# Performance work log

Hardware: AMD Instinct MI355X
Metric: run time of the kernel (lower is better)

Reference implementation:

```python
import jax, jax.numpy as jnp
import numpy as np

B, S, D_MODEL, N_HEADS = 2, 2048, 2048, 16
D_K = D_MODEL // N_HEADS
MAX_SEQ_LEN = 4096


def _rope_tables(seq_len, d_k):
    # matches RotaryPositionalEmbedding buffers
    inv_freq = 1.0 / (10000.0 ** (jnp.arange(0, d_k, 2, dtype=jnp.float32) / d_k))
    pos = jnp.arange(seq_len, dtype=jnp.float32)
    freqs = pos[:, None] * inv_freq[None, :]  # [S, d_k/2]
    return jnp.cos(freqs), jnp.sin(freqs)


def _apply_rope(x, cos, sin):
    # x: [B, H, S, d_k]; cos/sin: [S, d_k/2] -> broadcast [1,1,S,d_k/2]
    cos = cos[None, None, :, :]
    sin = sin[None, None, :, :]
    x_even = x[..., ::2]
    x_odd = x[..., 1::2]
    r_even = x_even * cos - x_odd * sin
    r_odd = x_even * sin + x_odd * cos
    return jnp.stack([r_even, r_odd], axis=-1).reshape(x.shape)


def setup_inputs() -> dict:
    key = jax.random.key(0)
    ks = jax.random.split(key, 5)
    scale = 1.0 / np.sqrt(D_MODEL)
    return {
        "x": jax.random.normal(ks[0], (B, S, D_MODEL), jnp.float32),
        "wq_w": jax.random.normal(ks[1], (D_MODEL, D_MODEL), jnp.float32) * scale,
        "wq_b": jnp.zeros((D_MODEL,), jnp.float32),
        "wk_w": jax.random.normal(ks[2], (D_MODEL, D_MODEL), jnp.float32) * scale,
        "wk_b": jnp.zeros((D_MODEL,), jnp.float32),
        "wv_w": jax.random.normal(ks[3], (D_MODEL, D_MODEL), jnp.float32) * scale,
        "wv_b": jnp.zeros((D_MODEL,), jnp.float32),
        "wo_w": jax.random.normal(ks[4], (D_MODEL, D_MODEL), jnp.float32) * scale,
        "wo_b": jnp.zeros((D_MODEL,), jnp.float32),
    }


def reference(x, wq_w, wq_b, wk_w, wk_b, wv_w, wv_b, wo_w, wo_b):
    b, s, _ = x.shape
    # QKV projections (torch Linear: x @ W.T + b), split heads -> [B, H, S, d_k]
    def proj(w, bias):
        y = jnp.einsum('bsd,ed->bse', x, w) + bias
        return y.reshape(b, s, N_HEADS, D_K).transpose(0, 2, 1, 3)

    q = proj(wq_w, wq_b)
    k = proj(wk_w, wk_b)
    v = proj(wv_w, wv_b)

    cos, sin = _rope_tables(s, D_K)
    q = _apply_rope(q, cos, sin)
    k = _apply_rope(k, cos, sin)

    # causal SDPA
    scale = 1.0 / np.sqrt(D_K).astype(np.float32)
    scores = jnp.einsum('bhqd,bhkd->bhqk', q, k) * scale
    causal = jnp.tril(jnp.ones((s, s), dtype=bool))
    scores = jnp.where(causal[None, None, :, :], scores, jnp.float32(-jnp.inf))
    attn = jax.nn.softmax(scores, axis=-1)
    out = jnp.einsum('bhqk,bhkd->bhqd', attn, v)

    out = out.transpose(0, 2, 1, 3).reshape(b, s, D_MODEL)
    return jnp.einsum('bsd,ed->bse', out, wo_w) + wo_b
```

## Files before the change

kernel.cpp:

```cpp
#include <hip/hip_runtime.h>


#define DMODEL 2048
#define SEQ    2048
#define NHEAD  16
#define DKH    128
#define NBATCH 2
#define MTOK   (NBATCH*SEQ)

typedef float  f32x4  __attribute__((ext_vector_type(4)));
typedef __bf16 bf16x8 __attribute__((ext_vector_type(8)));
typedef unsigned short      u16;
typedef unsigned short      u16x4 __attribute__((ext_vector_type(4)));

__device__ __forceinline__ float b2f(u16 u) {
    union { unsigned i; float f; } x; x.i = ((unsigned)u) << 16; return x.f;
}
__device__ __forceinline__ u16 f2bf(float f) {
    union { float f; unsigned i; } x; x.f = f;
    unsigned r = x.i + 0x7fffu + ((x.i >> 16) & 1u);
    return (u16)(r >> 16);
}

__device__ __forceinline__ void load_lds16(const void* g, void* l) {
    __builtin_amdgcn_global_load_lds(
        (const __attribute__((address_space(1))) void*)g,
        (__attribute__((address_space(3))) void*)l, 16, 0, 0);
}

__global__ void cast_f2b_kernel(const float* __restrict__ in, u16* __restrict__ out, int n4) {
    int i = blockIdx.x * blockDim.x + threadIdx.x;
    if (i >= n4) return;
    float4 f = ((const float4*)in)[i];
    uint2 o;
    o.x = (unsigned)f2bf(f.x) | ((unsigned)f2bf(f.y) << 16);
    o.y = (unsigned)f2bf(f.z) | ((unsigned)f2bf(f.w) << 16);
    ((uint2*)out)[i] = o;
}

template<int MODE>
__global__ __launch_bounds__(256) void gemm_bt(
    const u16* __restrict__ A, const u16* __restrict__ W,
    const float* __restrict__ bias, void* __restrict__ Cout,
    int M, int N, int K)
{
    __shared__ u16 As[128 * 64];
    __shared__ u16 Bs[128 * 64];
    const int tid  = threadIdx.x;
    const int lane = tid & 63;
    const int w    = tid >> 6;
    const int wm   = w >> 1, wn = w & 1;
    const int quad = lane >> 4, l16 = lane & 15;
    const int row0 = blockIdx.y * 128;
    const int col0 = blockIdx.x * 128;

    f32x4 acc[4][4] = {};

    for (int kt = 0; kt < K / 64; ++kt) {
        const int k0 = kt * 64;
#pragma unroll
        for (int i = 0; i < 4; ++i) {
            int cb = (i * 4 + w) * 64;
            int p  = cb + lane;
            int r  = p >> 3;
            int cl = (p & 7) ^ (r & 7);
            load_lds16(A + (size_t)(row0 + r) * K + k0 + cl * 8, (void*)(As + cb * 8));
            load_lds16(W + (size_t)(col0 + r) * K + k0 + cl * 8, (void*)(Bs + cb * 8));
        }
        __syncthreads();
#pragma unroll
        for (int ks = 0; ks < 2; ++ks) {
            bf16x8 af[4], bfr[4];
#pragma unroll
            for (int mi = 0; mi < 4; ++mi) {
                int r  = wm * 64 + mi * 16 + l16;
                int pc = (ks * 4 + quad) ^ (r & 7);
                af[mi] = *(const bf16x8*)(As + (r * 8 + pc) * 8);
            }
#pragma unroll
            for (int ni = 0; ni < 4; ++ni) {
                int r  = wn * 64 + ni * 16 + l16;
                int pc = (ks * 4 + quad) ^ (r & 7);
                bfr[ni] = *(const bf16x8*)(Bs + (r * 8 + pc) * 8);
            }
#pragma unroll
            for (int mi = 0; mi < 4; ++mi)
#pragma unroll
                for (int ni = 0; ni < 4; ++ni)
                    acc[mi][ni] = __builtin_amdgcn_mfma_f32_16x16x32_bf16(
                        af[mi], bfr[ni], acc[mi][ni], 0, 0, 0);
        }
        __syncthreads();
    }
#pragma unroll
    for (int mi = 0; mi < 4; ++mi) {
#pragma unroll
        for (int ni = 0; ni < 4; ++ni) {
            int col = col0 + wn * 64 + ni * 16 + l16;
            float bv = bias[col];
            if (MODE == 2) {
                int rowb = row0 + wm * 64 + mi * 16 + quad * 4;
                int bb = rowb >> 11, s = rowb & 2047;
                u16x4 pk;
#pragma unroll
                for (int r = 0; r < 4; ++r) pk[r] = f2bf(acc[mi][ni][r] + bv);
                *(u16x4*)((u16*)Cout + (size_t)(bb * 2048 + col) * 2048 + s) = pk;
            } else {
#pragma unroll
                for (int r = 0; r < 4; ++r) {
                    int row = row0 + wm * 64 + mi * 16 + quad * 4 + r;
                    float v = acc[mi][ni][r] + bv;
                    if (MODE == 1) ((u16*)Cout)[(size_t)row * N + col] = f2bf(v);
                    else           ((float*)Cout)[(size_t)row * N + col] = v;
                }
            }
        }
    }
}

__global__ void rope_kernel(u16* __restrict__ Q, u16* __restrict__ Kt) {
    int idx = blockIdx.x * blockDim.x + threadIdx.x;
    u16* P      = blockIdx.y ? Kt : Q;
    float scale = blockIdx.y ? 1.0f : 0.08838834764831845f;
    int i   = idx & 63;
    int tok = idx >> 10;
    int s   = tok & (SEQ - 1);
    unsigned pr = *(const unsigned*)(P + 2 * (size_t)idx);
    float e = b2f((u16)(pr & 0xffff)), o = b2f((u16)(pr >> 16));
    float inv_freq = exp2f(-13.287712379549449f * (float)i * (1.0f / 64.0f));
    float ang = (float)s * inv_freq;
    float c, sn;
    sincosf(ang, &sn, &c);
    float re = (e * c - o * sn) * scale;
    float ro = (e * sn + o * c) * scale;
    *(unsigned*)(P + 2 * (size_t)idx) = (unsigned)f2bf(re) | ((unsigned)f2bf(ro) << 16);
}

__global__ __launch_bounds__(512, 4) void attn_kernel(
    const u16* __restrict__ Q, const u16* __restrict__ Kg,
    const u16* __restrict__ VTg, u16* __restrict__ Out)
{
    const int p  = blockIdx.x;
    const int bh = blockIdx.y;
    const int b  = bh >> 4, h = bh & 15;

    const int tid  = threadIdx.x;
    const int lane = tid & 63;
    const int w    = tid >> 6;
    const int half = w >> 2;
    const int wsub = w & 3;
    const int quad = lane >> 4, l16 = lane & 15;

    const int q_hi  = 31 - p;
    const int my_qt = half ? q_hi : p;
    const int q0    = my_qt * 64;

    __shared__ u16 Ks[64 * 128];
    __shared__ u16 Vt[128 * 64];
    __shared__ u16 Ps[8][16 * 72];

    bf16x8 qf[4];
    const u16* qrow = Q + (size_t)(b * SEQ + q0 + wsub * 16 + l16) * DMODEL + h * DKH;
#pragma unroll
    for (int ks = 0; ks < 4; ++ks) qf[ks] = *(const bf16x8*)(qrow + ks * 32 + quad * 8);

    f32x4 o[8] = {};
    float m_r[4], l_r[4];
#pragma unroll
    for (int r = 0; r < 4; ++r) { m_r[r] = -1e30f; l_r[r] = 0.f; }

    for (int kt = 0; kt <= q_hi; ++kt) {
        const int k0 = kt * 64;
#pragma unroll
        for (int i = 0; i < 2; ++i) {
            int cb = (i * 8 + w) * 64;
            int pc = cb + lane;
            int r  = pc >> 4;
            int cl = (pc & 15) ^ (r & 15);
            load_lds16(Kg + (size_t)(b * SEQ + k0 + r) * DMODEL + h * DKH + cl * 8,
                       (void*)(Ks + cb * 8));
        }
#pragma unroll
        for (int i = 0; i < 2; ++i) {
            int cb = (i * 8 + w) * 64;
            int pc = cb + lane;
            int r  = pc >> 3;
            int cl = (pc & 7) ^ (r & 7);
            load_lds16(VTg + (size_t)(b * 2048 + h * DKH + r) * SEQ + k0 + cl * 8,
                       (void*)(Vt + cb * 8));
        }
        __syncthreads();

        if (kt <= my_qt) {
            f32x4 sc[4] = {};
#pragma unroll
            for (int ks = 0; ks < 4; ++ks) {
#pragma unroll
                for (int nt = 0; nt < 4; ++nt) {
                    int r  = nt * 16 + l16;
                    int pc = (ks * 4 + quad) ^ (r & 15);
                    bf16x8 kf = *(const bf16x8*)(Ks + (r * 16 + pc) * 8);
                    sc[nt] = __builtin_amdgcn_mfma_f32_16x16x32_bf16(qf[ks], kf, sc[nt], 0, 0, 0);
                }
            }
            if (kt == my_qt) {
#pragma unroll
                for (int nt = 0; nt < 4; ++nt)
#pragma unroll
                    for (int r = 0; r < 4; ++r) {
                        int col = k0 + nt * 16 + l16;
                        int row = q0 + wsub * 16 + quad * 4 + r;
                        if (col > row) sc[nt][r] = -1e30f;
                    }
            }
            float rmax[4] = { -1e30f, -1e30f, -1e30f, -1e30f };
#pragma unroll
            for (int nt = 0; nt < 4; ++nt)
#pragma unroll
                for (int r = 0; r < 4; ++r) rmax[r] = fmaxf(rmax[r], sc[nt][r]);
#pragma unroll
            for (int r = 0; r < 4; ++r)
#pragma unroll
                for (int off = 1; off < 16; off <<= 1)
                    rmax[r] = fmaxf(rmax[r], __shfl_xor(rmax[r], off));
            float alpha[4], rsum[4];
#pragma unroll
            for (int r = 0; r < 4; ++r) {
                float mnew = fmaxf(m_r[r], rmax[r]);
                alpha[r] = __expf(m_r[r] - mnew);
                m_r[r] = mnew;
                rsum[r] = 0.f;
            }
#pragma unroll
            for (int nt = 0; nt < 4; ++nt)
#pragma unroll
                for (int r = 0; r < 4; ++r) {
                    float pv = __expf(sc[nt][r] - m_r[r]);
                    rsum[r] += pv;
                    Ps[w][(quad * 4 + r) * 72 + nt * 16 + l16] = f2bf(pv);
                }
#pragma unroll
            for (int r = 0; r < 4; ++r) {
#pragma unroll
                for (int off = 1; off < 16; off <<= 1) rsum[r] += __shfl_xor(rsum[r], off);
                l_r[r] = l_r[r] * alpha[r] + rsum[r];
            }
#pragma unroll
            for (int nt = 0; nt < 8; ++nt)
#pragma unroll
                for (int r = 0; r < 4; ++r) o[nt][r] = o[nt][r] * alpha[r];

#pragma unroll
            for (int ks = 0; ks < 2; ++ks) {
                bf16x8 pf = *(const bf16x8*)(&Ps[w][l16 * 72 + ks * 32 + quad * 8]);
#pragma unroll
                for (int nt = 0; nt < 8; ++nt) {
                    int r  = nt * 16 + l16;
                    int pc = (ks * 4 + quad) ^ (r & 7);
                    bf16x8 vf = *(const bf16x8*)(Vt + r * 64 + pc * 8);
                    o[nt] = __builtin_amdgcn_mfma_f32_16x16x32_bf16(pf, vf, o[nt], 0, 0, 0);
                }
            }
        }
        __syncthreads();
    }

#pragma unroll
    for (int r = 0; r < 4; ++r) {
        float inv = 1.0f / l_r[r];
        int row = q0 + wsub * 16 + quad * 4 + r;
#pragma unroll
        for (int nt = 0; nt < 8; ++nt)
            Out[(size_t)(b * SEQ + row) * DMODEL + h * DKH + nt * 16 + l16] = f2bf(o[nt][r] * inv);
    }
}

extern "C" void kernel_launch(void* const* d_in, const int* in_sizes, int n_in,
                              void* d_out, int out_size, void* d_ws, size_t ws_size,
                              hipStream_t stream)
{
    const float* x    = (const float*)d_in[0];
    const float* wq_w = (const float*)d_in[1];
    const float* wq_b = (const float*)d_in[2];
    const float* wk_w = (const float*)d_in[3];
    const float* wk_b = (const float*)d_in[4];
    const float* wv_w = (const float*)d_in[5];
    const float* wv_b = (const float*)d_in[6];
    const float* wo_w = (const float*)d_in[7];
    const float* wo_b = (const float*)d_in[8];
    float* out = (float*)d_out;

    char* ws = (char*)d_ws;
    u16* XB  = (u16*)(ws);
    u16* WQB = (u16*)(ws + (16u << 20));
    u16* WKB = (u16*)(ws + (24u << 20));
    u16* WVB = (u16*)(ws + (32u << 20));
    u16* WOB = (u16*)(ws + (40u << 20));
    u16* QB  = (u16*)(ws + (48u << 20));
    u16* KB  = (u16*)(ws + (64u << 20));
    u16* VTB = (u16*)(ws + (80u << 20));

    cast_f2b_kernel<<<8192, 256, 0, stream>>>(x,    XB,  (MTOK * DMODEL) / 4);
    cast_f2b_kernel<<<4096, 256, 0, stream>>>(wq_w, WQB, (DMODEL * DMODEL) / 4);
    cast_f2b_kernel<<<4096, 256, 0, stream>>>(wk_w, WKB, (DMODEL * DMODEL) / 4);
    cast_f2b_kernel<<<4096, 256, 0, stream>>>(wv_w, WVB, (DMODEL * DMODEL) / 4);
    cast_f2b_kernel<<<4096, 256, 0, stream>>>(wo_w, WOB, (DMODEL * DMODEL) / 4);

    dim3 ggrid(DMODEL / 128, MTOK / 128);
    gemm_bt<1><<<ggrid, 256, 0, stream>>>(XB, WQB, wq_b, QB,  MTOK, DMODEL, DMODEL);
    gemm_bt<1><<<ggrid, 256, 0, stream>>>(XB, WKB, wk_b, KB,  MTOK, DMODEL, DMODEL);
    gemm_bt<2><<<ggrid, 256, 0, stream>>>(XB, WVB, wv_b, VTB, MTOK, DMODEL, DMODEL);

    rope_kernel<<<dim3((MTOK * NHEAD * 64) / 256, 2), 256, 0, stream>>>(QB, KB);

    attn_kernel<<<dim3(16, NBATCH * NHEAD), 512, 0, stream>>>(QB, KB, VTB, XB);

    gemm_bt<0><<<ggrid, 256, 0, stream>>>(XB, WOB, wo_b, out, MTOK, DMODEL, DMODEL);
}
```

Baseline: 437.0 us.

## Fuse QKV projections with RoPE epilogue, merge casts, use exp2 softmax

Concatenates Q/K/V weights into one buffer so a single GEMM computes all three projections. RoPE and the softmax scale (folded with log2 e) are applied in the GEMM epilogue via lane shuffles, removing the separate rope kernel. The five cast launches are merged into one 2D-grid launch, and the attention softmax uses a hardware exp2. Adds per-element sin/cos work in the epilogue and keeps scalar 16-bit stores for Q/K.

```diff
diff --git a/kernel.cpp b/kernel.cpp
--- a/kernel.cpp
+++ b/kernel.cpp
@@ -13,9 +13,19 @@
 typedef unsigned short      u16;
 typedef unsigned short      u16x4 __attribute__((ext_vector_type(4)));
 
-__device__ __forceinline__ float b2f(u16 u) {
-    union { unsigned i; float f; } x; x.i = ((unsigned)u) << 16; return x.f;
-}
+#if __has_builtin(__builtin_amdgcn_exp2f)
+#define EXP2F __builtin_amdgcn_exp2f
+#else
+#define EXP2F exp2f
+#endif
+#if __has_builtin(__builtin_amdgcn_sinf)
+#define SINR __builtin_amdgcn_sinf
+#define COSR __builtin_amdgcn_cosf
+#else
+__device__ __forceinline__ float SINR(float r){ return sinf(r * 6.283185307179586f); }
+__device__ __forceinline__ float COSR(float r){ return cosf(r * 6.283185307179586f); }
+#endif
+
 __device__ __forceinline__ u16 f2bf(float f) {
     union { float f; unsigned i; } x; x.f = f;
     unsigned r = x.i + 0x7fffu + ((x.i >> 16) & 1u);
@@ -28,20 +38,127 @@
         (__attribute__((address_space(3))) void*)l, 16, 0, 0);
 }
 
-__global__ void cast_f2b_kernel(const float* __restrict__ in, u16* __restrict__ out, int n4) {
+struct CastArgs {
+    const float* src[5];
+    u16*         dst[5];
+    int          n4[5];
+};
+__global__ void cast_all_kernel(CastArgs a) {
+    int j = blockIdx.y;
     int i = blockIdx.x * blockDim.x + threadIdx.x;
-    if (i >= n4) return;
-    float4 f = ((const float4*)in)[i];
+    if (i >= a.n4[j]) return;
+    float4 f = ((const float4*)a.src[j])[i];
     uint2 o;
     o.x = (unsigned)f2bf(f.x) | ((unsigned)f2bf(f.y) << 16);
     o.y = (unsigned)f2bf(f.z) | ((unsigned)f2bf(f.w) << 16);
-    ((uint2*)out)[i] = o;
-}
-
-template<int MODE>
-__global__ __launch_bounds__(256) void gemm_bt(
+    ((uint2*)a.dst[j])[i] = o;
+}
+
+__global__ __launch_bounds__(256) void gemm_qkv(
     const u16* __restrict__ A, const u16* __restrict__ W,
-    const float* __restrict__ bias, void* __restrict__ Cout,
+    const float* __restrict__ qb, const float* __restrict__ kb,
+    const float* __restrict__ vb,
+    u16* __restrict__ QB, u16* __restrict__ KB, u16* __restrict__ VT)
+{
+    __shared__ u16 As[128 * 64];
+    __shared__ u16 Bs[128 * 64];
+    const int tid  = threadIdx.x;
+    const int lane = tid & 63;
+    const int w    = tid >> 6;
+    const int wm   = w >> 1, wn = w & 1;
+    const int quad = lane >> 4, l16 = lane & 15;
+    const int row0 = blockIdx.y * 128;
+    const int col0 = blockIdx.x * 128;
+    const int K    = DMODEL;
+
+    f32x4 acc[4][4] = {};
+
+    for (int kt = 0; kt < K / 64; ++kt) {
+        const int k0 = kt * 64;
+#pragma unroll
+        for (int i = 0; i < 4; ++i) {
+            int cb = (i * 4 + w) * 64;
+            int p  = cb + lane;
+            int r  = p >> 3;
+            int cl = (p & 7) ^ (r & 7);
+            load_lds16(A + (size_t)(row0 + r) * K + k0 + cl * 8, (void*)(As + cb * 8));
+            load_lds16(W + (size_t)(col0 + r) * K + k0 + cl * 8, (void*)(Bs + cb * 8));
+        }
+        __syncthreads();
+#pragma unroll
+        for (int ks = 0; ks < 2; ++ks) {
+            bf16x8 af[4], bfr[4];
+#pragma unroll
+            for (int mi = 0; mi < 4; ++mi) {
+                int r  = wm * 64 + mi * 16 + l16;
+                int pc = (ks * 4 + quad) ^ (r & 7);
+                af[mi] = *(const bf16x8*)(As + (r * 8 + pc) * 8);
+            }
+#pragma unroll
+            for (int ni = 0; ni < 4; ++ni) {
+                int r  = wn * 64 + ni * 16 + l16;
+                int pc = (ks * 4 + quad) ^ (r & 7);
+                bfr[ni] = *(const bf16x8*)(Bs + (r * 8 + pc) * 8);
+            }
+#pragma unroll
+            for (int mi = 0; mi < 4; ++mi)
+#pragma unroll
+                for (int ni = 0; ni < 4; ++ni)
+                    acc[mi][ni] = __builtin_amdgcn_mfma_f32_16x16x32_bf16(
+                        af[mi], bfr[ni], acc[mi][ni], 0, 0, 0);
+        }
+        __syncthreads();
+    }
+
+    const int sect = col0 >> 11;
+    if (sect == 2) {
+#pragma unroll
+        for (int mi = 0; mi < 4; ++mi) {
+#pragma unroll
+            for (int ni = 0; ni < 4; ++ni) {
+                int colv = (col0 & 2047) + wn * 64 + ni * 16 + l16;
+                float bv = vb[colv];
+                int rowb = row0 + wm * 64 + mi * 16 + quad * 4;
+                int bb = rowb >> 11, s = rowb & 2047;
+                u16x4 pk;
+#pragma unroll
+                for (int r = 0; r < 4; ++r) pk[r] = f2bf(acc[mi][ni][r] + bv);
+                *(u16x4*)(VT + (size_t)(bb * 2048 + colv) * 2048 + s) = pk;
+            }
+        }
+    } else {
+        const float* bias = sect ? kb : qb;
+        u16* dst          = sect ? KB : QB;
+        const float rs = sect ? 1.0f : 0.1275174376f;
+#pragma unroll
+        for (int ni = 0; ni < 4; ++ni) {
+            int col = col0 + wn * 64 + ni * 16 + l16;
+            int d   = col & 127;
+            int fi  = d >> 1;
+            float invf_rev = exp2f(-0.2076205059304601f * (float)fi) * 0.15915494309189535f;
+            float bvv = bias[col & 2047];
+            float sgn = (col & 1) ? 1.0f : -1.0f;
+#pragma unroll
+            for (int mi = 0; mi < 4; ++mi) {
+#pragma unroll
+                for (int r = 0; r < 4; ++r) {
+                    int row = row0 + wm * 64 + mi * 16 + quad * 4 + r;
+                    float v  = acc[mi][ni][r] + bvv;
+                    float pv = __shfl_xor(v, 1);
+                    float rev = (float)(row & 2047) * invf_rev;
+                    rev -= floorf(rev);
+                    float cc = COSR(rev), ss = SINR(rev);
+                    float res = (cc * v + sgn * ss * pv) * rs;
+                    dst[(size_t)row * 2048 + (col & 2047)] = f2bf(res);
+                }
+            }
+        }
+    }
+}
+
+__global__ __launch_bounds__(256) void gemm_o(
+    const u16* __restrict__ A, const u16* __restrict__ W,
+    const float* __restrict__ bias, float* __restrict__ Cout,
     int M, int N, int K)
 {
     __shared__ u16 As[128 * 64];
@@ -98,42 +215,13 @@
         for (int ni = 0; ni < 4; ++ni) {
             int col = col0 + wn * 64 + ni * 16 + l16;
             float bv = bias[col];
-            if (MODE == 2) {
-                int rowb = row0 + wm * 64 + mi * 16 + quad * 4;
-                int bb = rowb >> 11, s = rowb & 2047;
-                u16x4 pk;
-#pragma unroll
-                for (int r = 0; r < 4; ++r) pk[r] = f2bf(acc[mi][ni][r] + bv);
-                *(u16x4*)((u16*)Cout + (size_t)(bb * 2048 + col) * 2048 + s) = pk;
-            } else {
-#pragma unroll
-                for (int r = 0; r < 4; ++r) {
-                    int row = row0 + wm * 64 + mi * 16 + quad * 4 + r;
-                    float v = acc[mi][ni][r] + bv;
-                    if (MODE == 1) ((u16*)Cout)[(size_t)row * N + col] = f2bf(v);
-                    else           ((float*)Cout)[(size_t)row * N + col] = v;
-                }
-            }
-        }
-    }
-}
-
-__global__ void rope_kernel(u16* __restrict__ Q, u16* __restrict__ Kt) {
-    int idx = blockIdx.x * blockDim.x + threadIdx.x;
-    u16* P      = blockIdx.y ? Kt : Q;
-    float scale = blockIdx.y ? 1.0f : 0.08838834764831845f;
-    int i   = idx & 63;
-    int tok = idx >> 10;
-    int s   = tok & (SEQ - 1);
-    unsigned pr = *(const unsigned*)(P + 2 * (size_t)idx);
-    float e = b2f((u16)(pr & 0xffff)), o = b2f((u16)(pr >> 16));
-    float inv_freq = exp2f(-13.287712379549449f * (float)i * (1.0f / 64.0f));
-    float ang = (float)s * inv_freq;
-    float c, sn;
-    sincosf(ang, &sn, &c);
-    float re = (e * c - o * sn) * scale;
-    float ro = (e * sn + o * c) * scale;
-    *(unsigned*)(P + 2 * (size_t)idx) = (unsigned)f2bf(re) | ((unsigned)f2bf(ro) << 16);
+#pragma unroll
+            for (int r = 0; r < 4; ++r) {
+                int row = row0 + wm * 64 + mi * 16 + quad * 4 + r;
+                Cout[(size_t)row * N + col] = acc[mi][ni][r] + bv;
+            }
+        }
+    }
 }
 
 __global__ __launch_bounds__(512, 4) void attn_kernel(
@@ -227,7 +315,7 @@
 #pragma unroll
             for (int r = 0; r < 4; ++r) {
                 float mnew = fmaxf(m_r[r], rmax[r]);
-                alpha[r] = __expf(m_r[r] - mnew);
+                alpha[r] = EXP2F(m_r[r] - mnew);
                 m_r[r] = mnew;
                 rsum[r] = 0.f;
             }
@@ -235,7 +323,7 @@
             for (int nt = 0; nt < 4; ++nt)
 #pragma unroll
                 for (int r = 0; r < 4; ++r) {
-                    float pv = __expf(sc[nt][r] - m_r[r]);
+                    float pv = EXP2F(sc[nt][r] - m_r[r]);
                     rsum[r] += pv;
                     Ps[w][(quad * 4 + r) * 72 + nt * 16 + l16] = f2bf(pv);
                 }
@@ -291,29 +379,24 @@
     float* out = (float*)d_out;
 
     char* ws = (char*)d_ws;
-    u16* XB  = (u16*)(ws);
-    u16* WQB = (u16*)(ws + (16u << 20));
-    u16* WKB = (u16*)(ws + (24u << 20));
-    u16* WVB = (u16*)(ws + (32u << 20));
-    u16* WOB = (u16*)(ws + (40u << 20));
-    u16* QB  = (u16*)(ws + (48u << 20));
-    u16* KB  = (u16*)(ws + (64u << 20));
-    u16* VTB = (u16*)(ws + (80u << 20));
-
-    cast_f2b_kernel<<<8192, 256, 0, stream>>>(x,    XB,  (MTOK * DMODEL) / 4);
-    cast_f2b_kernel<<<4096, 256, 0, stream>>>(wq_w, WQB, (DMODEL * DMODEL) / 4);
-    cast_f2b_kernel<<<4096, 256, 0, stream>>>(wk_w, WKB, (DMODEL * DMODEL) / 4);
-    cast_f2b_kernel<<<4096, 256, 0, stream>>>(wv_w, WVB, (DMODEL * DMODEL) / 4);
-    cast_f2b_kernel<<<4096, 256, 0, stream>>>(wo_w, WOB, (DMODEL * DMODEL) / 4);
-
-    dim3 ggrid(DMODEL / 128, MTOK / 128);
-    gemm_bt<1><<<ggrid, 256, 0, stream>>>(XB, WQB, wq_b, QB,  MTOK, DMODEL, DMODEL);
-    gemm_bt<1><<<ggrid, 256, 0, stream>>>(XB, WKB, wk_b, KB,  MTOK, DMODEL, DMODEL);
-    gemm_bt<2><<<ggrid, 256, 0, stream>>>(XB, WVB, wv_b, VTB, MTOK, DMODEL, DMODEL);
-
-    rope_kernel<<<dim3((MTOK * NHEAD * 64) / 256, 2), 256, 0, stream>>>(QB, KB);
+    u16* XB   = (u16*)(ws);
+    u16* WQKV = (u16*)(ws + (16u << 20));
+    u16* WOB  = (u16*)(ws + (40u << 20));
+    u16* QB   = (u16*)(ws + (48u << 20));
+    u16* KB   = (u16*)(ws + (64u << 20));
+    u16* VTB  = (u16*)(ws + (80u << 20));
+
+    CastArgs ca;
+    ca.src[0] = x;    ca.dst[0] = XB;                     ca.n4[0] = (MTOK * DMODEL) / 4;
+    ca.src[1] = wq_w; ca.dst[1] = WQKV;                   ca.n4[1] = (DMODEL * DMODEL) / 4;
+    ca.src[2] = wk_w; ca.dst[2] = WQKV + DMODEL * DMODEL; ca.n4[2] = (DMODEL * DMODEL) / 4;
+    ca.src[3] = wv_w; ca.dst[3] = WQKV + 2 * DMODEL * DMODEL; ca.n4[3] = (DMODEL * DMODEL) / 4;
+    ca.src[4] = wo_w; ca.dst[4] = WOB;                    ca.n4[4] = (DMODEL * DMODEL) / 4;
+    cast_all_kernel<<<dim3(8192, 5), 256, 0, stream>>>(ca);
+
+    gemm_qkv<<<dim3(48, 32), 256, 0, stream>>>(XB, WQKV, wq_b, wk_b, wv_b, QB, KB, VTB);
 
     attn_kernel<<<dim3(16, NBATCH * NHEAD), 512, 0, stream>>>(QB, KB, VTB, XB);
 
-    gemm_bt<0><<<ggrid, 256, 0, stream>>>(XB, WOB, wo_b, out, MTOK, DMODEL, DMODEL);
-}
+    gemm_o<<<dim3(16, 32), 256, 0, stream>>>(XB, WOB, wo_b, out, MTOK, DMODEL, DMODEL);
+}
```

After: 503.8 us. 1.15x slower.
